# Optimization experiments

Measured on AMD Instinct MI355X. Metric: run time of the kernel, lower is better.

The kernel has to match this reference:

```python
import jax, jax.numpy as jnp
import numpy as np
from jax import lax

DN = ('NCHW', 'OIHW', 'NCHW')

def conv3x3(x, w, b):
    y = lax.conv_general_dilated(x, w, (1, 1), 'SAME', dimension_numbers=DN)
    return y + b[None, :, None, None]

def box_filter(x, ws):
    # depthwise WxW averaging conv, VALID after reflect pad
    C = x.shape[1]
    k = jnp.ones((C, 1, ws, ws), x.dtype) / (ws * ws)
    return lax.conv_general_dilated(x, k, (1, 1), 'VALID', feature_group_count=C,
                                    dimension_numbers=DN)

def compute_std_map(features, ws):
    N, C, H, W = features.shape
    pad = ws // 2
    fp = jnp.pad(features, ((0, 0), (0, 0), (pad, pad), (pad, pad)), mode='reflect')
    local_mean = box_filter(fp, ws)            # [N,C,H,W]
    local_mean_sq = box_filter(fp * fp, ws)
    local_var = jnp.clip(local_mean_sq - local_mean ** 2, 1e-6, None)
    if C == 4:
        cw = jax.nn.softmax(jnp.array([1.0, 1.5, 1.0, 1.5], features.dtype))
    else:
        cw = jax.nn.softmax(jnp.ones((C,), features.dtype))
    result = jnp.sum(jnp.sqrt(local_var) * cw[None, :, None, None], axis=1, keepdims=True)
    return result ** 0.8                        # [N,1,H,W]

def setup_inputs() -> dict:
    key = jax.random.key(0)
    ks = jax.random.split(key, 10)
    inp = {}
    inp['x'] = jax.random.normal(ks[0], (1, 4, 1024, 1024), jnp.float32)
    inp['w1'] = jax.random.normal(ks[1], (32, 4, 3, 3), jnp.float32) * (1.0 / np.sqrt(4 * 9))
    inp['b1'] = jax.random.normal(ks[2], (32,), jnp.float32) * 0.01
    inp['w2'] = jax.random.normal(ks[3], (16, 32, 3, 3), jnp.float32) * (1.0 / np.sqrt(32 * 9))
    inp['b2'] = jax.random.normal(ks[4], (16,), jnp.float32) * 0.01
    inp['w3'] = jax.random.normal(ks[5], (8, 16, 3, 3), jnp.float32) * (1.0 / np.sqrt(16 * 9))
    inp['b3'] = jax.random.normal(ks[6], (8,), jnp.float32) * 0.01
    inp['channel_weights'] = jnp.ones((4,), jnp.float32) / 4.0
    inp['fusion_w'] = jnp.full((1, 3, 1, 1), 1.0 / 3.0, jnp.float32) + \
        jax.random.normal(ks[7], (1, 3, 1, 1), jnp.float32) * 0.02
    inp['fusion_b'] = jnp.zeros((1,), jnp.float32)
    return inp

def reference(x, w1, b1, w2, b2, w3, b3, channel_weights, fusion_w, fusion_b):
    window_sizes = [11, 25, 49]
    # feature extractor
    f = jax.nn.leaky_relu(conv3x3(x, w1, b1), 0.2)
    f = jax.nn.leaky_relu(conv3x3(f, w2, b2), 0.2)
    f = conv3x3(f, w3, b3)                      # [B,8,H,W]
    # multi-scale std maps
    maps = jnp.concatenate([compute_std_map(f, ws) for ws in window_sizes], axis=1)  # [B,3,H,W]
    fused = jax.nn.relu(
        lax.conv_general_dilated(maps, fusion_w, (1, 1), 'VALID', dimension_numbers=DN)
        + fusion_b[None, :, None, None])        # [B,1,H,W]
    # adaptive thresholds
    std_flat = fused.reshape(-1)
    q25 = jnp.quantile(std_flat, 0.25)
    q75 = jnp.quantile(std_flat, 0.75)
    iqr75 = q75 - q25
    global_std = jnp.std(x, axis=(2, 3), keepdims=True, ddof=1)   # [B,4,1,1]
    lower = (q25 - 0.5 * iqr75) * jnp.ones_like(global_std)
    upper = (q75 + 0.5 * iqr75) * jnp.ones_like(global_std)
    gf = jnp.clip(global_std * 5.0, 0.5, 2.0)
    lower = lower * gf
    upper = upper * gf
    cwn = jax.nn.softmax(channel_weights).reshape(1, 4, 1, 1)
    channel_std = jnp.std(x * cwn, axis=(2, 3), keepdims=True, ddof=1)
    cf = jnp.clip(channel_std * 2.0, 0.8, 1.2)
    lower = lower * cf
    upper = upper * cf
    # texture mask
    q30 = jnp.quantile(std_flat, 0.3)
    q70 = jnp.quantile(std_flat, 0.7)
    lower_mean = jnp.mean(lower, axis=1, keepdims=True)           # [B,1,1,1]
    upper_mean = jnp.mean(upper, axis=1, keepdims=True)
    l_t = 0.5 * lower_mean + 0.5 * q30
    u_t = 0.5 * upper_mean + 0.5 * q70
    iqr = q70 - q30
    widen = iqr < 0.01
    l_t = jnp.where(widen, l_t - iqr, l_t)
    u_t = jnp.where(widen, u_t + iqr, u_t)
    diff = u_t - l_t
    mid0 = (l_t + u_t) / 2
    narrow = diff < 0.02
    l_t = jnp.where(narrow, mid0 - 0.01, l_t)
    u_t = jnp.where(narrow, mid0 + 0.01, u_t)
    midpoint = (l_t + u_t) / 2
    scale = u_t - l_t
    normalized = jax.nn.sigmoid(4.0 * (fused - midpoint) / scale)
    nm = jnp.mean(normalized)
    mask = jnp.where(nm > 0.65, 0.1 + 0.5 * normalized,
                     jnp.where(nm < 0.35, 0.2 + 0.5 * normalized,
                               0.15 + 0.55 * normalized))
    return mask
```

## Files before the change

### kernel.cpp

```cpp
#include <hip/hip_runtime.h>
#include <stdint.h>

constexpr int H = 1024, W = 1024;
constexpr int NPIX = H * W;
constexpr int PADM = 24;
constexpr int PROW = W + 2 * PADM;

constexpr size_t OFF_F1P   = 0;
constexpr size_t OFF_F2P   = 134217728;
constexpr size_t OFF_F3    = 0;
constexpr size_t OFF_HF    = 33554432;
constexpr size_t OFF_HF2   = 67108864;
constexpr size_t OFF_FUSED = 100663296;
constexpr size_t OFF_HF25  = 134217728;
constexpr size_t OFF_HF225 = 167772160;
constexpr size_t OFF_SMALL  = 201326592;
constexpr size_t OFF_PSTAT  = OFF_SMALL;
constexpr size_t OFF_NMSUM  = OFF_SMALL + 4096;
constexpr size_t OFF_HIST   = OFF_SMALL + 4160;
constexpr size_t OFF_RSTATE = OFF_HIST + 8192;
constexpr size_t OFF_SCAL   = OFF_RSTATE + 64;
constexpr size_t OFF_H0     = OFF_SCAL + 64;
constexpr size_t OFF_WT     = OFF_H0 + 1024;

using short8  = __attribute__((ext_vector_type(8))) short;
using short4v = __attribute__((ext_vector_type(4))) short;
using f32x4   = __attribute__((ext_vector_type(4))) float;
using uint2v  = __attribute__((ext_vector_type(2))) unsigned int;
using uint4v  = __attribute__((ext_vector_type(4))) unsigned int;

__device__ __forceinline__ int reflect1024(int j) {
    return j < 0 ? -j : (j > 1023 ? 2046 - j : j);
}
__device__ __forceinline__ unsigned short rne_bf16(float v) {
    uint32_t u = __float_as_uint(v);
    return (unsigned short)((u + 0x7FFFu + ((u >> 16) & 1u)) >> 16);
}
__device__ __forceinline__ float bf16f(unsigned short h) {
    return __uint_as_float(((uint32_t)h) << 16);
}
__device__ __forceinline__ uint32_t pack_hl(float v) {
    uint32_t u = __float_as_uint(v);
    unsigned short hh = (unsigned short)(u >> 16);
    unsigned short ll = rne_bf16(v - __uint_as_float(u & 0xFFFF0000u));
    return (uint32_t)hh | ((uint32_t)ll << 16);
}

__device__ void wfrag_body(const float* __restrict__ w, unsigned short* __restrict__ wfH,
                           unsigned short* __restrict__ wfL, int CIN, int COUT, int NF, int S,
                           int blk) {
    int total = NF * S * 512;
    int e = blk * 256 + threadIdx.x;
    if (e >= total) return;
    int j = e & 7, l = (e >> 3) & 63;
    int rest = e >> 9;
    int s = rest % S, nf = rest / S;
    int k = s * 32 + ((l >> 4) << 3) + j;
    int n = (l & 15) + 16 * nf;
    float v = 0.f;
    if (k < 9 * CIN && n < COUT) {
        int kk = k / CIN, c = k % CIN;
        int ky = kk / 3, kx = kk - ky * 3;
        v = w[((n * CIN + c) * 3 + ky) * 3 + kx];
    }
    unsigned short h = rne_bf16(v);
    wfH[e] = h;
    wfL[e] = rne_bf16(v - bf16f(h));
}

__global__ void prep_kernel(const float* __restrict__ w1, const float* __restrict__ w2,
                            const float* __restrict__ w3,
                            unsigned short* wf1H, unsigned short* wf1L,
                            unsigned short* wf2H, unsigned short* wf2L,
                            unsigned short* wf3H, unsigned short* wf3L,
                            const float* __restrict__ x, double* __restrict__ pstats,
                            double* nmsum, uint32_t* hist, uint32_t* rstate,
                            uint32_t* h0) {
    __shared__ double sb1[256], sb2[256];
    const int b = blockIdx.x, tid = threadIdx.x;
    if (b == 0) {
        for (int i = tid; i < 2048; i += 256) hist[i] = 0u;
        h0[tid] = 0u;
        if (tid == 0) nmsum[0] = 0.0;
        if (tid < 8) rstate[tid] = 0u;
        if (tid < 8) {
            const uint32_t ranks[8] = {262143u, 262144u, 314572u, 314573u,
                                       734002u, 734003u, 786431u, 786432u};
            rstate[8 + tid] = ranks[tid];
        }
    } else if (b < 9) {
        wfrag_body(w1, wf1H, wf1L, 4, 32, 2, 2, b - 1);
    } else if (b < 27) {
        wfrag_body(w2, wf2H, wf2L, 32, 16, 1, 9, b - 9);
    } else if (b < 37) {
        wfrag_body(w3, wf3H, wf3L, 16, 8, 1, 5, b - 27);
    } else {
        int sb = b - 37;
        int ch = sb >> 6, blk = sb & 63;
        const float* p = x + (size_t)ch * NPIX;
        double s1 = 0.0, s2 = 0.0;
        for (int i = blk * 256 + tid; i < NPIX; i += 64 * 256) {
            double v = (double)p[i];
            s1 += v; s2 += v * v;
        }
        sb1[tid] = s1; sb2[tid] = s2;
        __syncthreads();
        for (int off = 128; off > 0; off >>= 1) {
            if (tid < off) { sb1[tid] += sb1[tid + off]; sb2[tid] += sb2[tid + off]; }
            __syncthreads();
        }
        if (tid == 0) { pstats[sb * 2] = sb1[0]; pstats[sb * 2 + 1] = sb2[0]; }
    }
}

template <int CIN, int COUT, int S, bool LEAKY, int OUT_MODE, int IN_MODE, int MINW>
__global__ __launch_bounds__(256, MINW) void mconv_kernel(
        const void* __restrict__ in,
        const unsigned short* __restrict__ wfH, const unsigned short* __restrict__ wfL,
        const float* __restrict__ bias, void* __restrict__ out) {
    constexpr int NF = (COUT + 15) / 16;
    constexpr int RS = 66 * CIN;
    constexpr int PSTR = COUT + 4;
    constexpr int STAGEB = 2 * (6 * RS) * 2;
    constexpr int EPIB = (OUT_MODE == 1) ? (4 * 64 * PSTR * 4) : (COUT * 4 * 66 * 4);
    constexpr int LBYTES = STAGEB > EPIB ? STAGEB : EPIB;
    __shared__ __align__(16) unsigned char LB[LBYTES];
    unsigned short* Ah = (unsigned short*)LB;
    unsigned short* Al = Ah + 6 * RS;

    const int tid = threadIdx.x;
    const int bx = blockIdx.x * 64, by = blockIdx.y * 4;
    const int lane = tid & 63, rw = tid >> 6;

    if constexpr (IN_MODE == 1) {
        constexpr int CPP = CIN / 4;
        constexpr int CROW = 66 * CPP;
        constexpr int TOT = 6 * CROW;
        constexpr int NLOAD = (TOT + 255) / 256;
        const uint32_t* gp = (const uint32_t*)in;

        uint4v regs[NLOAD];
#pragma unroll
        for (int k = 0; k < NLOAD; ++k) {
            int idx = tid + k * 256;
            uint4v v = uint4v{0u, 0u, 0u, 0u};
            if (idx < TOT) {
                int r = idx / CROW;
                int j = idx - r * CROW;
                int gy = by - 1 + r;
                int gx = bx - 1 + j / CPP;
                if ((unsigned)gy < 1024u && (unsigned)gx < 1024u)
                    v = *(const uint4v*)(gp + ((size_t)gy << 10) * CIN +
                                         (size_t)(bx - 1) * CIN + (size_t)j * 4);
            }
            regs[k] = v;
        }
#pragma unroll
        for (int k = 0; k < NLOAD; ++k) {
            int idx = tid + k * 256;
            if (idx < TOT) {
                int r = idx / CROW;
                int j = idx - r * CROW;
                int px = j / CPP, c0 = (j - px * CPP) * 4;
                uint32_t p0 = regs[k].x, p1 = regs[k].y, p2 = regs[k].z, p3 = regs[k].w;
                uint2v hh, ll;
                hh.x = __builtin_amdgcn_perm(p1, p0, 0x05040100u);
                hh.y = __builtin_amdgcn_perm(p3, p2, 0x05040100u);
                ll.x = __builtin_amdgcn_perm(p1, p0, 0x07060302u);
                ll.y = __builtin_amdgcn_perm(p3, p2, 0x07060302u);
                int off = r * RS + px * CIN + c0;
                *(uint2v*)(Ah + off) = hh;
                *(uint2v*)(Al + off) = ll;
            }
        }
    } else {
        constexpr int TOT = 6 * 4 * 66;
        constexpr int NLOAD = (TOT + 255) / 256;
        const float* xin = (const float*)in;
        float regs[NLOAD];
#pragma unroll
        for (int k = 0; k < NLOAD; ++k) {
            int idx = tid + k * 256;
            float v = 0.f;
            if (idx < TOT) {
                int rc  = idx / 66;
                int px  = idx - rc * 66;
                int r   = rc >> 2, c = rc & 3;
                int gy = by - 1 + r, gx = bx - 1 + px;
                if ((unsigned)gy < 1024u && (unsigned)gx < 1024u)
                    v = xin[(size_t)c * NPIX + ((size_t)gy << 10) + gx];
            }
            regs[k] = v;
        }
#pragma unroll
        for (int k = 0; k < NLOAD; ++k) {
            int idx = tid + k * 256;
            if (idx < TOT) {
                int rc  = idx / 66;
                int px  = idx - rc * 66;
                int r   = rc >> 2, c = rc & 3;
                uint32_t u = __float_as_uint(regs[k]);
                Ah[r * RS + px * CIN + c] = (unsigned short)(u >> 16);
                Al[r * RS + px * CIN + c] =
                    rne_bf16(regs[k] - __uint_as_float(u & 0xFFFF0000u));
            }
        }
    }

    short8 wh[NF][S], wl[NF][S];
#pragma unroll
    for (int nf = 0; nf < NF; ++nf)
#pragma unroll
        for (int s = 0; s < S; ++s) {
            wh[nf][s] = *(const short8*)(wfH + (size_t)((nf * S + s) * 64 + lane) * 8);
            wl[nf][s] = *(const short8*)(wfL + (size_t)((nf * S + s) * 64 + lane) * 8);
        }

    const int nidx = lane & 15;
    f32x4 acc[4][NF];
#pragma unroll
    for (int nf = 0; nf < NF; ++nf) {
        float bv = (nidx + nf * 16 < COUT) ? bias[nidx + nf * 16] : 0.f;
#pragma unroll
        for (int t = 0; t < 4; ++t) acc[t][nf] = f32x4{bv, bv, bv, bv};
    }

    __syncthreads();

    if constexpr (CIN == 32) {
        const int base = rw * RS + (lane & 15) * 32 + (lane >> 4) * 8;
        const unsigned short* pah = Ah + base;
        const unsigned short* pal = Al + base;
#pragma unroll
        for (int s = 0; s < S; ++s) {
            const int ky = s / 3, kx = s - (s / 3) * 3;
#pragma unroll
            for (int t = 0; t < 4; ++t) {
                const int off = ky * RS + kx * 32 + t * 512;
                short8 a = *(const short8*)(pah + off);
                short8 b = *(const short8*)(pal + off);
#pragma unroll
                for (int nf = 0; nf < NF; ++nf) {
                    acc[t][nf] = __builtin_amdgcn_mfma_f32_16x16x32_bf16(a, wh[nf][s], acc[t][nf], 0, 0, 0);
                    acc[t][nf] = __builtin_amdgcn_mfma_f32_16x16x32_bf16(b, wh[nf][s], acc[t][nf], 0, 0, 0);
                    acc[t][nf] = __builtin_amdgcn_mfma_f32_16x16x32_bf16(a, wl[nf][s], acc[t][nf], 0, 0, 0);
                }
            }
        }
    } else if constexpr (CIN == 16) {
        const int g23 = lane >> 5;
        const int base = rw * RS + (lane & 15) * 16 + ((lane >> 4) & 1) * 8;
#pragma unroll
        for (int s = 0; s < S; ++s) {
            const int kk0 = 2 * s, kk1 = 2 * s + 1;
            const int O0 = (kk0 / 3) * RS + (kk0 - (kk0 / 3) * 3) * 16;
            const int O1 = (kk1 <= 8) ? (kk1 / 3) * RS + (kk1 - (kk1 / 3) * 3) * 16 : 0;
            const int offs = base + (g23 ? O1 : O0);
#pragma unroll
            for (int t = 0; t < 4; ++t) {
                short8 a = *(const short8*)(Ah + offs + t * 256);
                short8 b = *(const short8*)(Al + offs + t * 256);
#pragma unroll
                for (int nf = 0; nf < NF; ++nf) {
                    acc[t][nf] = __builtin_amdgcn_mfma_f32_16x16x32_bf16(a, wh[nf][s], acc[t][nf], 0, 0, 0);
                    acc[t][nf] = __builtin_amdgcn_mfma_f32_16x16x32_bf16(b, wh[nf][s], acc[t][nf], 0, 0, 0);
                    acc[t][nf] = __builtin_amdgcn_mfma_f32_16x16x32_bf16(a, wl[nf][s], acc[t][nf], 0, 0, 0);
                }
            }
        }
    } else {
        const int base = rw * RS + (lane & 15) * 4;
        const int g2 = (lane >> 4) * 2;
#pragma unroll
        for (int s = 0; s < S; ++s) {
            int kkA = s * 8 + g2, kkB = kkA + 1;
            int kyA = (kkA * 11) >> 5; int kxA = kkA - kyA * 3;
            int poA = (kkA <= 8) ? kyA * RS + kxA * 4 : 0;
            int kyB = (kkB * 11) >> 5; int kxB = kkB - kyB * 3;
            int poB = (kkB <= 8) ? kyB * RS + kxB * 4 : 0;
#pragma unroll
            for (int t = 0; t < 4; ++t) {
                union { short4v q[2]; short8 o; } ua, ub;
                ua.q[0] = *(const short4v*)(Ah + base + poA + t * 64);
                ua.q[1] = *(const short4v*)(Ah + base + poB + t * 64);
                ub.q[0] = *(const short4v*)(Al + base + poA + t * 64);
                ub.q[1] = *(const short4v*)(Al + base + poB + t * 64);
                short8 a = ua.o, b = ub.o;
#pragma unroll
                for (int nf = 0; nf < NF; ++nf) {
                    acc[t][nf] = __builtin_amdgcn_mfma_f32_16x16x32_bf16(a, wh[nf][s], acc[t][nf], 0, 0, 0);
                    acc[t][nf] = __builtin_amdgcn_mfma_f32_16x16x32_bf16(b, wh[nf][s], acc[t][nf], 0, 0, 0);
                    acc[t][nf] = __builtin_amdgcn_mfma_f32_16x16x32_bf16(a, wl[nf][s], acc[t][nf], 0, 0, 0);
                }
            }
        }
    }

    const int mrow = (lane >> 4) * 4;
    if constexpr (OUT_MODE == 0) {
        __syncthreads();
        float* smem = (float*)LB;
        if (nidx < COUT) {
#pragma unroll
            for (int t = 0; t < 4; ++t)
#pragma unroll
                for (int j = 0; j < 4; ++j) {
                    float v = acc[t][0][j];
                    if (LEAKY) v = v >= 0.f ? v : 0.2f * v;
                    smem[(nidx * 4 + rw) * 66 + t * 16 + mrow + j] = v;
                }
        }
        __syncthreads();
        float* outp = (float*)out;
#pragma unroll
        for (int k = 0; k < COUT; ++k) {
            int i = tid + k * 256;
            int px = i & 63, r = (i >> 6) & 3, c = i >> 8;
            outp[(size_t)c * NPIX + ((size_t)(by + r) << 10) + bx + px] =
                smem[(c * 4 + r) * 66 + px];
        }
    } else {
        __syncthreads();
        uint32_t* pk = (uint32_t*)LB;
#pragma unroll
        for (int t = 0; t < 4; ++t)
#pragma unroll
            for (int nf = 0; nf < NF; ++nf)
#pragma unroll
                for (int j = 0; j < 4; ++j) {
                    float v = acc[t][nf][j];
                    if (LEAKY) v = v >= 0.f ? v : 0.2f * v;
                    int xl = t * 16 + mrow + j;
                    pk[(rw * 64 + xl) * PSTR + nf * 16 + nidx] = pack_hl(v);
                }
        __syncthreads();
        uint32_t* gp = (uint32_t*)out;
        constexpr int ROWU = 64 * COUT;
        constexpr int NU4 = 4 * ROWU / 4;
#pragma unroll
        for (int k = 0; k < (NU4 + 255) / 256; ++k) {
            int i = tid + k * 256;
            if (i < NU4) {
                int e = i * 4;
                int r = e / ROWU;
                int rem = e - r * ROWU;
                int px = rem / COUT, c = rem - px * COUT;
                uint4v val = *(const uint4v*)&pk[(r * 64 + px) * PSTR + c];
                *(uint4v*)(gp + ((size_t)(((by + r) << 10) + bx + px)) * COUT + c) = val;
            }
        }
    }
}

template <bool DOB>
__global__ void hbox_kernel(const float* __restrict__ f3,
                            float* __restrict__ hfA, float* __restrict__ hf2A, int pA,
                            float* __restrict__ hfB, float* __restrict__ hf2B, int pB) {
    const int row = blockIdx.x, ch = blockIdx.y, tid = threadIdx.x;
    const float* src = f3 + ch * NPIX + row * W;
    __shared__ float sraw[PROW];
    __shared__ float Pf[PROW + 1], Pf2[PROW + 1];
    __shared__ float wtot[4], wtot2[4];

    for (int i = tid; i < PROW; i += 256)
        sraw[i] = src[reflect1024(i - PADM)];
    __syncthreads();

    float lf[5], lf2[5];
    float sf = 0.f, sf2 = 0.f;
    const int base = tid * 5;
#pragma unroll
    for (int j = 0; j < 5; ++j) {
        int idx = base + j;
        float v = (idx < PROW) ? sraw[idx] : 0.f;
        sf += v;      lf[j] = sf;
        sf2 += v * v; lf2[j] = sf2;
    }
    const int lane = tid & 63, wid = tid >> 6;
    float tf = sf, tf2 = sf2;
#pragma unroll
    for (int off = 1; off < 64; off <<= 1) {
        float a = __shfl_up(tf, off);
        float b = __shfl_up(tf2, off);
        if (lane >= off) { tf += a; tf2 += b; }
    }
    if (lane == 63) { wtot[wid] = tf; wtot2[wid] = tf2; }
    __syncthreads();
    float bse = 0.f, bse2 = 0.f;
    for (int w2 = 0; w2 < wid; ++w2) { bse += wtot[w2]; bse2 += wtot2[w2]; }
    float ex = bse + tf - sf, ex2 = bse2 + tf2 - sf2;
    if (base <= PROW) { Pf[base] = ex; Pf2[base] = ex2; }
#pragma unroll
    for (int j = 0; j < 5; ++j) {
        int idx = base + j + 1;
        if (idx <= PROW) { Pf[idx] = ex + lf[j]; Pf2[idx] = ex2 + lf2[j]; }
    }
    __syncthreads();

    float* dfA  = hfA  + ch * NPIX + row * W;
    float* df2A = hf2A + ch * NPIX + row * W;
    float* dfB  = DOB ? (hfB  + ch * NPIX + row * W) : nullptr;
    float* df2B = DOB ? (hf2B + ch * NPIX + row * W) : nullptr;
    for (int x = tid; x < W; x += 256) {
        int a = x + PADM - pA, b = x + PADM + pA + 1;
        dfA[x]  = Pf[b]  - Pf[a];
        df2A[x] = Pf2[b] - Pf2[a];
        if (DOB) {
            int a2 = x + PADM - pB, b2 = x + PADM + pB + 1;
            dfB[x]  = Pf[b2]  - Pf[a2];
            df2B[x] = Pf2[b2] - Pf2[a2];
        }
    }
}

template <int VRSP, bool DOH>
__global__ __launch_bounds__(512) void vbox_kernel(const float* __restrict__ hf,
                                                   const float* __restrict__ hf2,
                                                   float* __restrict__ fused,
                                                   const float* __restrict__ fw,
                                                   const float* __restrict__ fb,
                                                   uint32_t* __restrict__ h0,
                                                   int kidx, int p, float inv_area) {
    const int tid = threadIdx.x;
    const int colIdx = tid & 63, ch = tid >> 6;
    const int col = blockIdx.x * 64 + colIdx;
    const int r0 = blockIdx.y * VRSP;
    const float* pf  = hf  + ch * NPIX + col;
    const float* pf2 = hf2 + ch * NPIX + col;

    __shared__ float ssq[8][8][65];
    __shared__ uint32_t lh[8][256];
    if (DOH) {
        for (int i = tid; i < 2048; i += 512) ((uint32_t*)lh)[i] = 0u;
    }

    float S1 = 0.f, S2 = 0.f;
    for (int t = -p; t <= p; ++t) {
        int rr = reflect1024(r0 + t);
        S1 += pf[rr * W];
        S2 += pf2[rr * W];
    }

    const float w = fw[kidx];
    const float bias0 = fb[0];
    const int jj = tid >> 6, cc = tid & 63;
    const int sub = jj;

    for (int rb = r0; rb < r0 + VRSP; rb += 8) {
#pragma unroll
        for (int j = 0; j < 8; ++j) {
            int r = rb + j;
            float m1 = S1 * inv_area, m2 = S2 * inv_area;
            float var = fmaxf(m2 - m1 * m1, 1e-6f);
            ssq[ch][j][colIdx] = sqrtf(var);
            int radd = reflect1024(r + 1 + p), rsub = reflect1024(r - p);
            S1 += pf[radd * W] - pf[rsub * W];
            S2 += pf2[radd * W] - pf2[rsub * W];
        }
        __syncthreads();
        float a = 0.f;
#pragma unroll
        for (int c8 = 0; c8 < 8; ++c8) a += ssq[c8][jj][cc];
        float m = powf(a * 0.125f, 0.8f);
        float* fp = fused + ((size_t)(rb + jj) << 10) + blockIdx.x * 64 + cc;
        float outv;
        if (kidx == 0)      { outv = bias0 + w * m; *fp = outv; }
        else if (kidx == 1) { outv = *fp + w * m;   *fp = outv; }
        else                { outv = fmaxf(*fp + w * m, 0.f); *fp = outv; }
        if (DOH) {
            uint32_t u = __float_as_uint(outv);
            uint32_t key = (u & 0x80000000u) ? ~u : (u | 0x80000000u);
            atomicAdd(&lh[sub][key >> 24], 1u);
        }
        __syncthreads();
    }

    if (DOH) {
        __syncthreads();
        if (tid < 256) {
            uint32_t v = 0;
#pragma unroll
            for (int s = 0; s < 8; ++s) v += lh[s][tid];
            if (v) atomicAdd(&h0[tid], v);
        }
    }
}

__global__ void radix_hist_kernel(const float* __restrict__ fused, uint32_t* __restrict__ hist,
                                  const uint32_t* __restrict__ rstate, int pass) {
    __shared__ uint32_t h[8][256];
    int tid = threadIdx.x;
    for (int i = tid; i < 2048; i += 256) ((uint32_t*)h)[i] = 0u;
    __syncthreads();

    uint32_t pref[8];
#pragma unroll
    for (int r = 0; r < 8; ++r) pref[r] = rstate[r];
    uint32_t maskHi = 0xFFFFFFFFu << (32 - 8 * pass);
    int shift = 24 - 8 * pass;

    const uint4v* fp4 = (const uint4v*)fused;
    for (int i = blockIdx.x * blockDim.x + tid; i < NPIX / 4; i += gridDim.x * blockDim.x) {
        uint4v u4 = fp4[i];
#pragma unroll
        for (int e = 0; e < 4; ++e) {
            uint32_t u = (e == 0) ? u4.x : (e == 1) ? u4.y : (e == 2) ? u4.z : u4.w;
            uint32_t key = (u & 0x80000000u) ? ~u : (u | 0x80000000u);
            uint32_t bin = (key >> shift) & 0xFFu;
#pragma unroll
            for (int r = 0; r < 8; ++r) {
                if (((key ^ pref[r]) & maskHi) == 0u)
                    atomicAdd(&h[r][bin], 1u);
            }
        }
    }
    __syncthreads();
    for (int i = tid; i < 2048; i += 256) {
        uint32_t v = ((uint32_t*)h)[i];
        if (v) atomicAdd(&hist[i], v);
    }
}

__device__ __forceinline__ float key_to_float(uint32_t k) {
    uint32_t u = (k & 0x80000000u) ? (k & 0x7FFFFFFFu) : ~k;
    return __uint_as_float(u);
}

__global__ void radix_scan_kernel(uint32_t* __restrict__ hist, uint32_t* __restrict__ rstate,
                                  int pass, const uint32_t* __restrict__ h0,
                                  const double* __restrict__ pstats,
                                  const float* __restrict__ cw, float* __restrict__ scal) {
    int tid = threadIdx.x;
    int shift = 24 - 8 * pass;
    const int lane = tid & 63, wv = tid >> 6;
    __shared__ uint32_t wsum[4];
    __shared__ uint32_t fkey[8];
    for (int r = 0; r < 8; ++r) {
        uint32_t c = (pass == 0) ? h0[tid] : hist[r * 256 + tid];
        uint32_t sc = c;
#pragma unroll
        for (int off = 1; off < 64; off <<= 1) {
            uint32_t t = __shfl_up(sc, off);
            if (lane >= off) sc += t;
        }
        if (lane == 63) wsum[wv] = sc;
        __syncthreads();
        uint32_t base = 0;
        for (int w2 = 0; w2 < wv; ++w2) base += wsum[w2];
        uint32_t incl = base + sc, excl = incl - c;
        uint32_t lr = rstate[8 + r];
        if (lr >= excl && lr < incl) {
            uint32_t nk = rstate[r] | (((uint32_t)tid) << shift);
            rstate[r] = nk;
            rstate[8 + r] = lr - excl;
            if (pass == 3) fkey[r] = nk;
        }
        if (pass > 0) hist[r * 256 + tid] = 0u;
        __syncthreads();
    }

    if (pass == 3) {
        double s1 = pstats[2 * tid], s2 = pstats[2 * tid + 1];
#pragma unroll
        for (int off = 32; off > 0; off >>= 1) {
            s1 += __shfl_down(s1, off);
            s2 += __shfl_down(s2, off);
        }
        __shared__ double gs[4][2];
        if ((tid & 63) == 0) { gs[tid >> 6][0] = s1; gs[tid >> 6][1] = s2; }
        __syncthreads();
        if (tid == 0) {
            float v[8];
#pragma unroll
            for (int r = 0; r < 8; ++r) v[r] = key_to_float(fkey[r]);
            float q25 = v[0] + 0.75f * (v[1] - v[0]);
            float q30 = v[2] + 0.5f * (v[3] - v[2]);
            float q70 = v[4] + 0.5f * (v[5] - v[4]);
            float q75 = v[6] + 0.25f * (v[7] - v[6]);

            const double N = (double)NPIX;
            float gstd[4];
#pragma unroll
            for (int c = 0; c < 4; ++c) {
                double a1 = gs[c][0], a2 = gs[c][1];
                double var = (a2 - a1 * a1 / N) / (N - 1.0);
                gstd[c] = (float)sqrt(var > 0.0 ? var : 0.0);
            }
            float m = fmaxf(fmaxf(cw[0], cw[1]), fmaxf(cw[2], cw[3]));
            float e0 = expf(cw[0] - m), e1 = expf(cw[1] - m);
            float e2 = expf(cw[2] - m), e3 = expf(cw[3] - m);
            float se = e0 + e1 + e2 + e3;
            float cwn[4] = {e0 / se, e1 / se, e2 / se, e3 / se};

            float iqr75 = q75 - q25;
            float low0 = q25 - 0.5f * iqr75;
            float up0  = q75 + 0.5f * iqr75;
            float lsum = 0.f, usum = 0.f;
#pragma unroll
            for (int c = 0; c < 4; ++c) {
                float gf = fminf(fmaxf(gstd[c] * 5.f, 0.5f), 2.f);
                float cs = cwn[c] * gstd[c];
                float cf = fminf(fmaxf(cs * 2.f, 0.8f), 1.2f);
                lsum += low0 * gf * cf;
                usum += up0 * gf * cf;
            }
            float lmean = 0.25f * lsum, umean = 0.25f * usum;
            float l_t = 0.5f * lmean + 0.5f * q30;
            float u_t = 0.5f * umean + 0.5f * q70;
            float iqr = q70 - q30;
            if (iqr < 0.01f) { l_t -= iqr; u_t += iqr; }
            float diff = u_t - l_t;
            float mid0 = 0.5f * (l_t + u_t);
            if (diff < 0.02f) { l_t = mid0 - 0.01f; u_t = mid0 + 0.01f; }
            scal[0] = 0.5f * (l_t + u_t);
            scal[1] = u_t - l_t;
        }
    }
}

__global__ void sigmoid_kernel(const float* __restrict__ fused, const float* __restrict__ scal,
                               double* __restrict__ nmsum) {
    float mid = scal[0], sc = scal[1];
    float inv = 4.0f / sc;
    float local = 0.f;
    const f32x4* fp4 = (const f32x4*)fused;
    for (int i = blockIdx.x * blockDim.x + threadIdx.x; i < NPIX / 4; i += gridDim.x * blockDim.x) {
        f32x4 v = fp4[i];
#pragma unroll
        for (int e = 0; e < 4; ++e) {
            float t = (v[e] - mid) * inv;
            local += 1.0f / (1.0f + expf(-t));
        }
    }
    __shared__ float red[256];
    red[threadIdx.x] = local;
    __syncthreads();
    for (int off = 128; off > 0; off >>= 1) {
        if (threadIdx.x < off) red[threadIdx.x] += red[threadIdx.x + off];
        __syncthreads();
    }
    if (threadIdx.x == 0) atomicAdd(nmsum, (double)red[0]);
}

__global__ void final_kernel(const float* __restrict__ fused, const float* __restrict__ scal,
                             const double* __restrict__ nmsum, float* __restrict__ out) {
    float nm = (float)(nmsum[0] / (double)NPIX);
    float a, b;
    if (nm > 0.65f)      { a = 0.10f; b = 0.50f; }
    else if (nm < 0.35f) { a = 0.20f; b = 0.50f; }
    else                 { a = 0.15f; b = 0.55f; }
    float mid = scal[0], inv = 4.0f / scal[1];
    const f32x4* fp4 = (const f32x4*)fused;
    f32x4* op4 = (f32x4*)out;
    for (int i = blockIdx.x * blockDim.x + threadIdx.x; i < NPIX / 4; i += gridDim.x * blockDim.x) {
        f32x4 v = fp4[i];
        f32x4 r;
#pragma unroll
        for (int e = 0; e < 4; ++e) {
            float t = (v[e] - mid) * inv;
            float n = 1.0f / (1.0f + expf(-t));
            r[e] = a + b * n;
        }
        op4[i] = r;
    }
}

extern "C" void kernel_launch(void* const* d_in, const int* in_sizes, int n_in,
                              void* d_out, int out_size, void* d_ws, size_t ws_size,
                              hipStream_t stream) {
    const float* x   = (const float*)d_in[0];
    const float* w1  = (const float*)d_in[1];
    const float* b1  = (const float*)d_in[2];
    const float* w2  = (const float*)d_in[3];
    const float* b2  = (const float*)d_in[4];
    const float* w3  = (const float*)d_in[5];
    const float* b3  = (const float*)d_in[6];
    const float* cw  = (const float*)d_in[7];
    const float* fw  = (const float*)d_in[8];
    const float* fb  = (const float*)d_in[9];

    char* ws = (char*)d_ws;
    uint32_t* f1p = (uint32_t*)(ws + OFF_F1P);
    uint32_t* f2p = (uint32_t*)(ws + OFF_F2P);
    float* f3    = (float*)(ws + OFF_F3);
    float* hf    = (float*)(ws + OFF_HF);
    float* hf2   = (float*)(ws + OFF_HF2);
    float* hf25  = (float*)(ws + OFF_HF25);
    float* hf225 = (float*)(ws + OFF_HF225);
    float* fused = (float*)(ws + OFF_FUSED);
    double* pstats = (double*)(ws + OFF_PSTAT);
    double* nmsum  = (double*)(ws + OFF_NMSUM);
    uint32_t* hist   = (uint32_t*)(ws + OFF_HIST);
    uint32_t* rstate = (uint32_t*)(ws + OFF_RSTATE);
    float* scal = (float*)(ws + OFF_SCAL);
    uint32_t* h0 = (uint32_t*)(ws + OFF_H0);
    unsigned short* wf1H = (unsigned short*)(ws + OFF_WT);
    unsigned short* wf1L = wf1H + 2048;
    unsigned short* wf2H = wf1L + 2048;
    unsigned short* wf2L = wf2H + 4608;
    unsigned short* wf3H = wf2L + 4608;
    unsigned short* wf3L = wf3H + 2560;

    prep_kernel<<<293, 256, 0, stream>>>(w1, w2, w3, wf1H, wf1L, wf2H, wf2L, wf3H, wf3L,
                                         x, pstats, nmsum, hist, rstate, h0);

    dim3 cgrid(16, 256);
    mconv_kernel<4, 32, 2, true, 1, 0, 4><<<cgrid, 256, 0, stream>>>(
        x, wf1H, wf1L, b1, f1p);
    mconv_kernel<32, 16, 9, true, 1, 1, 3><<<cgrid, 256, 0, stream>>>(
        f1p, wf2H, wf2L, b2, f2p);
    mconv_kernel<16, 8, 5, false, 0, 1, 4><<<cgrid, 256, 0, stream>>>(
        f2p, wf3H, wf3L, b3, f3);

    hbox_kernel<true><<<dim3(H, 8), 256, 0, stream>>>(f3, hf, hf2, 5, hf25, hf225, 12);
    vbox_kernel<32, false><<<dim3(16, 32), 512, 0, stream>>>(hf, hf2, fused, fw, fb,
                                                             nullptr, 0, 5, 1.0f / 121.0f);
    hbox_kernel<false><<<dim3(H, 8), 256, 0, stream>>>(f3, hf, hf2, 24,
                                                       nullptr, nullptr, 0);
    vbox_kernel<32, false><<<dim3(16, 32), 512, 0, stream>>>(hf25, hf225, fused, fw, fb,
                                                             nullptr, 1, 12, 1.0f / 625.0f);
    vbox_kernel<64, true><<<dim3(16, 16), 512, 0, stream>>>(hf, hf2, fused, fw, fb,
                                                            h0, 2, 24, 1.0f / 2401.0f);

    radix_scan_kernel<<<1, 256, 0, stream>>>(hist, rstate, 0, h0, pstats, cw, scal);
    for (int pass = 1; pass < 4; ++pass) {
        radix_hist_kernel<<<1024, 256, 0, stream>>>(fused, hist, rstate, pass);
        radix_scan_kernel<<<1, 256, 0, stream>>>(hist, rstate, pass, h0, pstats, cw, scal);
    }

    sigmoid_kernel<<<1024, 256, 0, stream>>>(fused, scal, nmsum);
    final_kernel<<<1024, 256, 0, stream>>>(fused, scal, nmsum, (float*)d_out);
}
```

Before: 346.3 us.

## Fuse first two conv layers into one kernel keeping conv1 output in LDS

Adds mconv12_kernel, which loads a 4-pixel halo of x, computes conv1 for the 6x66 tile needed by conv2 directly into shared memory as split bf16 hi/lo, and then runs conv2 from LDS. This removes the 32-channel f1 intermediate write and read through global memory (about 128MB each way) and one kernel launch. In exchange it recomputes conv1 on halo rows and columns (396 vs 256 pixels per tile), uses more LDS per block, which limits occupancy to 2 blocks, and adds a serial dependency between the two phases within each block. The generic mconv kernel is simplified to the CIN=16 path only.

```diff
diff --git a/kernel.cpp b/kernel.cpp
--- a/kernel.cpp
+++ b/kernel.cpp
@@ -6,7 +6,6 @@
 constexpr int PADM = 24;
 constexpr int PROW = W + 2 * PADM;
 
-constexpr size_t OFF_F1P   = 0;
 constexpr size_t OFF_F2P   = 134217728;
 constexpr size_t OFF_F3    = 0;
 constexpr size_t OFF_HF    = 33554432;
@@ -113,16 +112,189 @@
     }
 }
 
-template <int CIN, int COUT, int S, bool LEAKY, int OUT_MODE, int IN_MODE, int MINW>
+__global__ __launch_bounds__(256, 2) void mconv12_kernel(
+        const float* __restrict__ x,
+        const unsigned short* __restrict__ wf1H, const unsigned short* __restrict__ wf1L,
+        const float* __restrict__ b1,
+        const unsigned short* __restrict__ wf2H, const unsigned short* __restrict__ wf2L,
+        const float* __restrict__ b2, uint32_t* __restrict__ out) {
+    constexpr int XRS = 68 * 4;
+    constexpr int RS  = 66 * 32;
+    constexpr int PSTR = 16 + 4;
+    __shared__ __align__(16) unsigned short Xh[8 * XRS], Xl[8 * XRS];
+    __shared__ __align__(16) unsigned short Ah[6 * RS], Al[6 * RS];
+
+    const int tid = threadIdx.x;
+    const int bx = blockIdx.x * 64, by = blockIdx.y * 4;
+    const int lane = tid & 63, rw = tid >> 6;
+    const int nidx = lane & 15;
+    const int mrow = (lane >> 4) * 4;
+
+    {
+        constexpr int TOT = 8 * 4 * 68;
+        constexpr int NLOAD = (TOT + 255) / 256;
+        float regs[NLOAD];
+#pragma unroll
+        for (int k = 0; k < NLOAD; ++k) {
+            int idx = tid + k * 256;
+            float v = 0.f;
+            if (idx < TOT) {
+                int rc = idx / 68, sp = idx - rc * 68;
+                int r = rc >> 2, c = rc & 3;
+                int gy = by - 2 + r, gx = bx - 2 + sp;
+                if ((unsigned)gy < 1024u && (unsigned)gx < 1024u)
+                    v = x[(size_t)c * NPIX + ((size_t)gy << 10) + gx];
+            }
+            regs[k] = v;
+        }
+#pragma unroll
+        for (int k = 0; k < NLOAD; ++k) {
+            int idx = tid + k * 256;
+            if (idx < TOT) {
+                int rc = idx / 68, sp = idx - rc * 68;
+                int r = rc >> 2, c = rc & 3;
+                uint32_t u = __float_as_uint(regs[k]);
+                Xh[r * XRS + sp * 4 + c] = (unsigned short)(u >> 16);
+                Xl[r * XRS + sp * 4 + c] =
+                    rne_bf16(regs[k] - __uint_as_float(u & 0xFFFF0000u));
+            }
+        }
+    }
+
+    short8 w1h[2][2], w1l[2][2];
+#pragma unroll
+    for (int nf = 0; nf < 2; ++nf)
+#pragma unroll
+        for (int s = 0; s < 2; ++s) {
+            w1h[nf][s] = *(const short8*)(wf1H + (size_t)((nf * 2 + s) * 64 + lane) * 8);
+            w1l[nf][s] = *(const short8*)(wf1L + (size_t)((nf * 2 + s) * 64 + lane) * 8);
+        }
+    short8 w2h[9], w2l[9];
+#pragma unroll
+    for (int s = 0; s < 9; ++s) {
+        w2h[s] = *(const short8*)(wf2H + (size_t)(s * 64 + lane) * 8);
+        w2l[s] = *(const short8*)(wf2L + (size_t)(s * 64 + lane) * 8);
+    }
+    const float b1v0 = b1[nidx], b1v1 = b1[nidx + 16];
+    const float b2v = b2[nidx];
+
+    __syncthreads();
+
+    const int g2 = (lane >> 4) * 2;
+#pragma unroll 1
+    for (int tt = 0; tt < 7; ++tt) {
+        int mt = rw + 4 * tt;
+        if (mt >= 25) break;
+        int m = mt * 16 + nidx;
+        int mm = (m < 396) ? m : 0;
+        int fr = mm / 66, fp = mm - fr * 66;
+        f32x4 a1[2];
+        a1[0] = f32x4{b1v0, b1v0, b1v0, b1v0};
+        a1[1] = f32x4{b1v1, b1v1, b1v1, b1v1};
+#pragma unroll
+        for (int s = 0; s < 2; ++s) {
+            int kkA = s * 8 + g2, kkB = kkA + 1;
+            int poA = (kkA <= 8) ? ((fr + kkA / 3) * XRS + (fp + kkA % 3) * 4)
+                                 : (fr * XRS + fp * 4);
+            int poB = (kkB <= 8) ? ((fr + kkB / 3) * XRS + (fp + kkB % 3) * 4)
+                                 : (fr * XRS + fp * 4);
+            union { short4v q[2]; short8 o; } ua, ub;
+            ua.q[0] = *(const short4v*)(Xh + poA);
+            ua.q[1] = *(const short4v*)(Xh + poB);
+            ub.q[0] = *(const short4v*)(Xl + poA);
+            ub.q[1] = *(const short4v*)(Xl + poB);
+            short8 a = ua.o, b = ub.o;
+#pragma unroll
+            for (int nf = 0; nf < 2; ++nf) {
+                a1[nf] = __builtin_amdgcn_mfma_f32_16x16x32_bf16(a, w1h[nf][s], a1[nf], 0, 0, 0);
+                a1[nf] = __builtin_amdgcn_mfma_f32_16x16x32_bf16(b, w1h[nf][s], a1[nf], 0, 0, 0);
+                a1[nf] = __builtin_amdgcn_mfma_f32_16x16x32_bf16(a, w1l[nf][s], a1[nf], 0, 0, 0);
+            }
+        }
+#pragma unroll
+        for (int j = 0; j < 4; ++j) {
+            int mo = mt * 16 + mrow + j;
+            if (mo < 396) {
+                int ofr = mo / 66, ofp = mo - ofr * 66;
+                int ay = by - 1 + ofr, ax = bx - 1 + ofp;
+                bool inimg = ((unsigned)ay < 1024u) && ((unsigned)ax < 1024u);
+#pragma unroll
+                for (int nf = 0; nf < 2; ++nf) {
+                    float v = a1[nf][j];
+                    v = v >= 0.f ? v : 0.2f * v;
+                    if (!inimg) v = 0.f;
+                    uint32_t u = __float_as_uint(v);
+                    unsigned short hh = (unsigned short)(u >> 16);
+                    int off = ofr * RS + ofp * 32 + nf * 16 + nidx;
+                    Ah[off] = hh;
+                    Al[off] = rne_bf16(v - __uint_as_float(u & 0xFFFF0000u));
+                }
+            }
+        }
+    }
+
+    f32x4 acc[4];
+#pragma unroll
+    for (int t = 0; t < 4; ++t) acc[t] = f32x4{b2v, b2v, b2v, b2v};
+
+    __syncthreads();
+
+    {
+        const int base = rw * RS + nidx * 32 + (lane >> 4) * 8;
+        const unsigned short* pah = Ah + base;
+        const unsigned short* pal = Al + base;
+#pragma unroll
+        for (int s = 0; s < 9; ++s) {
+            const int ky = s / 3, kx = s - (s / 3) * 3;
+#pragma unroll
+            for (int t = 0; t < 4; ++t) {
+                const int off = ky * RS + kx * 32 + t * 512;
+                short8 a = *(const short8*)(pah + off);
+                short8 b = *(const short8*)(pal + off);
+                acc[t] = __builtin_amdgcn_mfma_f32_16x16x32_bf16(a, w2h[s], acc[t], 0, 0, 0);
+                acc[t] = __builtin_amdgcn_mfma_f32_16x16x32_bf16(b, w2h[s], acc[t], 0, 0, 0);
+                acc[t] = __builtin_amdgcn_mfma_f32_16x16x32_bf16(a, w2l[s], acc[t], 0, 0, 0);
+            }
+        }
+    }
+
+    __syncthreads();
+    uint32_t* pk = (uint32_t*)Ah;
+#pragma unroll
+    for (int t = 0; t < 4; ++t)
+#pragma unroll
+        for (int j = 0; j < 4; ++j) {
+            float v = acc[t][j];
+            v = v >= 0.f ? v : 0.2f * v;
+            int xl = t * 16 + mrow + j;
+            pk[(rw * 64 + xl) * PSTR + nidx] = pack_hl(v);
+        }
+    __syncthreads();
+    {
+        constexpr int ROWU = 64 * 16;
+        constexpr int NU4 = 4 * ROWU / 4;
+#pragma unroll
+        for (int k = 0; k < NU4 / 256; ++k) {
+            int i = tid + k * 256;
+            int e = i * 4;
+            int r = e / ROWU;
+            int rem = e - r * ROWU;
+            int px = rem / 16, c = rem - px * 16;
+            uint4v val = *(const uint4v*)&pk[(r * 64 + px) * PSTR + c];
+            *(uint4v*)(out + ((size_t)(((by + r) << 10) + bx + px)) * 16 + c) = val;
+        }
+    }
+}
+
+template <int CIN, int COUT, int S, bool LEAKY, int MINW>
 __global__ __launch_bounds__(256, MINW) void mconv_kernel(
         const void* __restrict__ in,
         const unsigned short* __restrict__ wfH, const unsigned short* __restrict__ wfL,
         const float* __restrict__ bias, void* __restrict__ out) {
     constexpr int NF = (COUT + 15) / 16;
     constexpr int RS = 66 * CIN;
-    constexpr int PSTR = COUT + 4;
     constexpr int STAGEB = 2 * (6 * RS) * 2;
-    constexpr int EPIB = (OUT_MODE == 1) ? (4 * 64 * PSTR * 4) : (COUT * 4 * 66 * 4);
+    constexpr int EPIB = COUT * 4 * 66 * 4;
     constexpr int LBYTES = STAGEB > EPIB ? STAGEB : EPIB;
     __shared__ __align__(16) unsigned char LB[LBYTES];
     unsigned short* Ah = (unsigned short*)LB;
@@ -132,7 +304,7 @@
     const int bx = blockIdx.x * 64, by = blockIdx.y * 4;
     const int lane = tid & 63, rw = tid >> 6;
 
-    if constexpr (IN_MODE == 1) {
+    {
         constexpr int CPP = CIN / 4;
         constexpr int CROW = 66 * CPP;
         constexpr int TOT = 6 * CROW;
@@ -173,38 +345,6 @@
                 *(uint2v*)(Al + off) = ll;
             }
         }
-    } else {
-        constexpr int TOT = 6 * 4 * 66;
-        constexpr int NLOAD = (TOT + 255) / 256;
-        const float* xin = (const float*)in;
-        float regs[NLOAD];
-#pragma unroll
-        for (int k = 0; k < NLOAD; ++k) {
-            int idx = tid + k * 256;
-            float v = 0.f;
-            if (idx < TOT) {
-                int rc  = idx / 66;
-                int px  = idx - rc * 66;
-                int r   = rc >> 2, c = rc & 3;
-                int gy = by - 1 + r, gx = bx - 1 + px;
-                if ((unsigned)gy < 1024u && (unsigned)gx < 1024u)
-                    v = xin[(size_t)c * NPIX + ((size_t)gy << 10) + gx];
-            }
-            regs[k] = v;
-        }
-#pragma unroll
-        for (int k = 0; k < NLOAD; ++k) {
-            int idx = tid + k * 256;
-            if (idx < TOT) {
-                int rc  = idx / 66;
-                int px  = idx - rc * 66;
-                int r   = rc >> 2, c = rc & 3;
-                uint32_t u = __float_as_uint(regs[k]);
-                Ah[r * RS + px * CIN + c] = (unsigned short)(u >> 16);
-                Al[r * RS + px * CIN + c] =
-                    rne_bf16(regs[k] - __uint_as_float(u & 0xFFFF0000u));
-            }
-        }
     }
 
     short8 wh[NF][S], wl[NF][S];
@@ -227,18 +367,19 @@
 
     __syncthreads();
 
-    if constexpr (CIN == 32) {
-        const int base = rw * RS + (lane & 15) * 32 + (lane >> 4) * 8;
-        const unsigned short* pah = Ah + base;
-        const unsigned short* pal = Al + base;
+    {
+        const int g23 = lane >> 5;
+        const int base = rw * RS + (lane & 15) * 16 + ((lane >> 4) & 1) * 8;
 #pragma unroll
         for (int s = 0; s < S; ++s) {
-            const int ky = s / 3, kx = s - (s / 3) * 3;
+            const int kk0 = 2 * s, kk1 = 2 * s + 1;
+            const int O0 = (kk0 / 3) * RS + (kk0 - (kk0 / 3) * 3) * 16;
+            const int O1 = (kk1 <= 8) ? (kk1 / 3) * RS + (kk1 - (kk1 / 3) * 3) * 16 : 0;
+            const int offs = base + (g23 ? O1 : O0);
 #pragma unroll
             for (int t = 0; t < 4; ++t) {
-                const int off = ky * RS + kx * 32 + t * 512;
-                short8 a = *(const short8*)(pah + off);
-                short8 b = *(const short8*)(pal + off);
+                short8 a = *(const short8*)(Ah + offs + t * 256);
+                short8 b = *(const short8*)(Al + offs + t * 256);
 #pragma unroll
                 for (int nf = 0; nf < NF; ++nf) {
                     acc[t][nf] = __builtin_amdgcn_mfma_f32_16x16x32_bf16(a, wh[nf][s], acc[t][nf], 0, 0, 0);
@@ -247,108 +388,29 @@
                 }
             }
         }
-    } else if constexpr (CIN == 16) {
-        const int g23 = lane >> 5;
-        const int base = rw * RS + (lane & 15) * 16 + ((lane >> 4) & 1) * 8;
-#pragma unroll
-        for (int s = 0; s < S; ++s) {
-            const int kk0 = 2 * s, kk1 = 2 * s + 1;
-            const int O0 = (kk0 / 3) * RS + (kk0 - (kk0 / 3) * 3) * 16;
-            const int O1 = (kk1 <= 8) ? (kk1 / 3) * RS + (kk1 - (kk1 / 3) * 3) * 16 : 0;
-            const int offs = base + (g23 ? O1 : O0);
-#pragma unroll
-            for (int t = 0; t < 4; ++t) {
-                short8 a = *(const short8*)(Ah + offs + t * 256);
-                short8 b = *(const short8*)(Al + offs + t * 256);
-#pragma unroll
-                for (int nf = 0; nf < NF; ++nf) {
-                    acc[t][nf] = __builtin_amdgcn_mfma_f32_16x16x32_bf16(a, wh[nf][s], acc[t][nf], 0, 0, 0);
-                    acc[t][nf] = __builtin_amdgcn_mfma_f32_16x16x32_bf16(b, wh[nf][s], acc[t][nf], 0, 0, 0);
-                    acc[t][nf] = __builtin_amdgcn_mfma_f32_16x16x32_bf16(a, wl[nf][s], acc[t][nf], 0, 0, 0);
-                }
-            }
-        }
-    } else {
-        const int base = rw * RS + (lane & 15) * 4;
-        const int g2 = (lane >> 4) * 2;
-#pragma unroll
-        for (int s = 0; s < S; ++s) {
-            int kkA = s * 8 + g2, kkB = kkA + 1;
-            int kyA = (kkA * 11) >> 5; int kxA = kkA - kyA * 3;
-            int poA = (kkA <= 8) ? kyA * RS + kxA * 4 : 0;
-            int kyB = (kkB * 11) >> 5; int kxB = kkB - kyB * 3;
-            int poB = (kkB <= 8) ? kyB * RS + kxB * 4 : 0;
-#pragma unroll
-            for (int t = 0; t < 4; ++t) {
-                union { short4v q[2]; short8 o; } ua, ub;
-                ua.q[0] = *(const short4v*)(Ah + base + poA + t * 64);
-                ua.q[1] = *(const short4v*)(Ah + base + poB + t * 64);
-                ub.q[0] = *(const short4v*)(Al + base + poA + t * 64);
-                ub.q[1] = *(const short4v*)(Al + base + poB + t * 64);
-                short8 a = ua.o, b = ub.o;
-#pragma unroll
-                for (int nf = 0; nf < NF; ++nf) {
-                    acc[t][nf] = __builtin_amdgcn_mfma_f32_16x16x32_bf16(a, wh[nf][s], acc[t][nf], 0, 0, 0);
-                    acc[t][nf] = __builtin_amdgcn_mfma_f32_16x16x32_bf16(b, wh[nf][s], acc[t][nf], 0, 0, 0);
-                    acc[t][nf] = __builtin_amdgcn_mfma_f32_16x16x32_bf16(a, wl[nf][s], acc[t][nf], 0, 0, 0);
-                }
-            }
-        }
     }
 
     const int mrow = (lane >> 4) * 4;
-    if constexpr (OUT_MODE == 0) {
-        __syncthreads();
-        float* smem = (float*)LB;
-        if (nidx < COUT) {
-#pragma unroll
-            for (int t = 0; t < 4; ++t)
-#pragma unroll
-                for (int j = 0; j < 4; ++j) {
-                    float v = acc[t][0][j];
-                    if (LEAKY) v = v >= 0.f ? v : 0.2f * v;
-                    smem[(nidx * 4 + rw) * 66 + t * 16 + mrow + j] = v;
-                }
-        }
-        __syncthreads();
-        float* outp = (float*)out;
-#pragma unroll
-        for (int k = 0; k < COUT; ++k) {
-            int i = tid + k * 256;
-            int px = i & 63, r = (i >> 6) & 3, c = i >> 8;
-            outp[(size_t)c * NPIX + ((size_t)(by + r) << 10) + bx + px] =
-                smem[(c * 4 + r) * 66 + px];
-        }
-    } else {
-        __syncthreads();
-        uint32_t* pk = (uint32_t*)LB;
+    __syncthreads();
+    float* smem = (float*)LB;
+    if (nidx < COUT) {
 #pragma unroll
         for (int t = 0; t < 4; ++t)
 #pragma unroll
-            for (int nf = 0; nf < NF; ++nf)
-#pragma unroll
-                for (int j = 0; j < 4; ++j) {
-                    float v = acc[t][nf][j];
-                    if (LEAKY) v = v >= 0.f ? v : 0.2f * v;
-                    int xl = t * 16 + mrow + j;
-                    pk[(rw * 64 + xl) * PSTR + nf * 16 + nidx] = pack_hl(v);
-                }
-        __syncthreads();
-        uint32_t* gp = (uint32_t*)out;
-        constexpr int ROWU = 64 * COUT;
-        constexpr int NU4 = 4 * ROWU / 4;
-#pragma unroll
-        for (int k = 0; k < (NU4 + 255) / 256; ++k) {
-            int i = tid + k * 256;
-            if (i < NU4) {
-                int e = i * 4;
-                int r = e / ROWU;
-                int rem = e - r * ROWU;
-                int px = rem / COUT, c = rem - px * COUT;
-                uint4v val = *(const uint4v*)&pk[(r * 64 + px) * PSTR + c];
-                *(uint4v*)(gp + ((size_t)(((by + r) << 10) + bx + px)) * COUT + c) = val;
-            }
-        }
+            for (int j = 0; j < 4; ++j) {
+                float v = acc[t][0][j];
+                if (LEAKY) v = v >= 0.f ? v : 0.2f * v;
+                smem[(nidx * 4 + rw) * 66 + t * 16 + mrow + j] = v;
+            }
+    }
+    __syncthreads();
+    float* outp = (float*)out;
+#pragma unroll
+    for (int k = 0; k < COUT; ++k) {
+        int i = tid + k * 256;
+        int px = i & 63, r = (i >> 6) & 3, c = i >> 8;
+        outp[(size_t)c * NPIX + ((size_t)(by + r) << 10) + bx + px] =
+            smem[(c * 4 + r) * 66 + px];
     }
 }
 
@@ -680,7 +742,6 @@
     const float* fb  = (const float*)d_in[9];
 
     char* ws = (char*)d_ws;
-    uint32_t* f1p = (uint32_t*)(ws + OFF_F1P);
     uint32_t* f2p = (uint32_t*)(ws + OFF_F2P);
     float* f3    = (float*)(ws + OFF_F3);
     float* hf    = (float*)(ws + OFF_HF);
@@ -705,11 +766,8 @@
                                          x, pstats, nmsum, hist, rstate, h0);
 
     dim3 cgrid(16, 256);
-    mconv_kernel<4, 32, 2, true, 1, 0, 4><<<cgrid, 256, 0, stream>>>(
-        x, wf1H, wf1L, b1, f1p);
-    mconv_kernel<32, 16, 9, true, 1, 1, 3><<<cgrid, 256, 0, stream>>>(
-        f1p, wf2H, wf2L, b2, f2p);
-    mconv_kernel<16, 8, 5, false, 0, 1, 4><<<cgrid, 256, 0, stream>>>(
+    mconv12_kernel<<<cgrid, 256, 0, stream>>>(x, wf1H, wf1L, b1, wf2H, wf2L, b2, f2p);
+    mconv_kernel<16, 8, 5, false, 4><<<cgrid, 256, 0, stream>>>(
         f2p, wf3H, wf3L, b3, f3);
 
     hbox_kernel<true><<<dim3(H, 8), 256, 0, stream>>>(f3, hf, hf2, 5, hf25, hf225, 12);
```

Measured after the change: 349.4 us. No clear change (+0.9%).
